# Performance work log

Hardware: AMD Instinct MI355X
Metric: run time of the kernel (lower is better)

Reference implementation:

```python
import jax, jax.numpy as jnp
import numpy as np

B, S, ENC_U, DEC_U, IN_DIM = 128, 1024, 1024, 1024, 64


def setup_inputs() -> dict:
    key = jax.random.key(0)
    ks = jax.random.split(key, 16)
    g = lambda k, shape, fan_in: jax.random.normal(k, shape, jnp.float32) / np.sqrt(fan_in)
    inp = {
        'x': jax.random.normal(ks[0], (B, 1, IN_DIM), jnp.float32),
        'hidden': jax.random.normal(ks[1], (B, DEC_U), jnp.float32),
        'enc_output': jax.random.normal(ks[2], (B, S, ENC_U), jnp.float32),
        # attention params
        'W1': g(ks[3], (ENC_U, DEC_U), ENC_U), 'b1': jnp.zeros((DEC_U,), jnp.float32),
        'W2': g(ks[4], (DEC_U, DEC_U), DEC_U), 'b2': jnp.zeros((DEC_U,), jnp.float32),
        'V': g(ks[5], (DEC_U, 1), DEC_U), 'bV': jnp.zeros((1,), jnp.float32),
        # GRU params (keras gate order: z, r, h); input to GRU is [context; x] -> ENC_U+IN_DIM
        'Wk': g(ks[6], (ENC_U + IN_DIM, 3 * DEC_U), ENC_U + IN_DIM),
        'Wr': g(ks[7], (DEC_U, 3 * DEC_U), DEC_U),
        'bg': jnp.zeros((3 * DEC_U,), jnp.float32),
        # output projection
        'Wfc': g(ks[8], (DEC_U, IN_DIM), DEC_U), 'bfc': jnp.zeros((IN_DIM,), jnp.float32),
    }
    return inp


def reference(x, hidden, enc_output, W1, b1, W2, b2, V, bV, Wk, Wr, bg, Wfc, bfc):
    U = hidden.shape[-1]
    # --- Bahdanau additive attention ---
    # score: (B, S, 1)
    feat = jnp.tanh(enc_output @ W1 + b1 + (hidden @ W2 + b2)[:, None, :])
    score = feat @ V + bV
    attention_weights = jax.nn.softmax(score, axis=1)            # (B, S, 1)
    context = jnp.sum(attention_weights * enc_output, axis=1)    # (B, ENC_U)
    # --- concat context with decoder input (single step) ---
    gin = jnp.concatenate([context, x[:, 0, :]], axis=-1)        # (B, ENC_U+IN_DIM)
    # --- one GRU cell step (reset_after=False, gate order z,r,h) ---
    xg = gin @ Wk + bg                                           # (B, 3U)
    z = jax.nn.sigmoid(xg[:, :U] + hidden @ Wr[:, :U])
    r = jax.nn.sigmoid(xg[:, U:2 * U] + hidden @ Wr[:, U:2 * U])
    hh = jnp.tanh(xg[:, 2 * U:] + (r * hidden) @ Wr[:, 2 * U:])
    state = z * hidden + (1.0 - z) * hh                          # (B, U)
    # return_sequences output with T=1 reshaped to (B, U) then fc
    out = state @ Wfc + bfc                                      # (B, IN_DIM)
    return out, state, attention_weights
```

## Files before the change

kernel.cpp:

```cpp
#include <hip/hip_runtime.h>
#include <cstdint>

#define B_  128
#define S_  1024
#define U_  1024
#define IN_ 64

typedef unsigned short u16;
typedef __attribute__((ext_vector_type(8))) short short8v;
typedef __attribute__((ext_vector_type(4))) float f32x4;

__device__ __forceinline__ u16 f2bf(float f) {
  uint32_t u = __builtin_bit_cast(uint32_t, f);
  u += 0x7fffu + ((u >> 16) & 1u);
  return (u16)(u >> 16);
}
__device__ __forceinline__ float bf2f(u16 h) {
  uint32_t u = ((uint32_t)h) << 16;
  return __builtin_bit_cast(float, u);
}
__device__ __forceinline__ float fast_tanh(float x) {
  float e = __expf(2.0f * x);
  return 1.0f - 2.0f * __builtin_amdgcn_rcpf(e + 1.0f);
}

__global__ void conv_enc_k(const float* __restrict__ in, u16* __restrict__ out) {
  size_t tid = (size_t)blockIdx.x * blockDim.x + threadIdx.x;
  size_t stride = (size_t)gridDim.x * blockDim.x;
  const size_t n8 = (size_t)B_ * S_ * U_ / 8;
  for (size_t p = tid; p < n8; p += stride) {
    const float* src = in + p * 8;
    float4 a = *(const float4*)src;
    float4 b = *(const float4*)(src + 4);
    short8v h;
    h[0] = (short)f2bf(a.x); h[1] = (short)f2bf(a.y);
    h[2] = (short)f2bf(a.z); h[3] = (short)f2bf(a.w);
    h[4] = (short)f2bf(b.x); h[5] = (short)f2bf(b.y);
    h[6] = (short)f2bf(b.z); h[7] = (short)f2bf(b.w);
    *(short8v*)(out + p * 8) = h;
  }
}

__global__ void conv_w1t_k(const float* __restrict__ W1, u16* __restrict__ w1t) {
  __shared__ float tile[32][33];
  int tx = threadIdx.x & 31, tg = threadIdx.x >> 5;
  int nb = blockIdx.x << 5, kb = blockIdx.y << 5;
#pragma unroll
  for (int i = 0; i < 4; ++i)
    tile[tg + i * 8][tx] = W1[(size_t)(kb + tg + i * 8) * U_ + nb + tx];
  __syncthreads();
#pragma unroll
  for (int i = 0; i < 4; ++i)
    w1t[(size_t)(nb + tg + i * 8) * U_ + kb + tx] = f2bf(tile[tx][tg + i * 8]);
}

__global__ __launch_bounds__(512, 2) void score_gemm2_k(
    const u16* __restrict__ encb, const u16* __restrict__ w1t,
    const float* __restrict__ hb, const float* __restrict__ b1,
    const float* __restrict__ b2, const float* __restrict__ Vv,
    float* __restrict__ score)
{
  __shared__ __align__(16) char lds[131072];
  const int tid  = threadIdx.x;
  const int lane = tid & 63;
  const int wid  = tid >> 6;
  const int wm = wid >> 2, wn = wid & 3;
  const int r16 = lane & 15, g4 = lane >> 4;

  int bid = blockIdx.x;
  int logical = (bid & 7) * 256 + (bid >> 3);
  const int row0 = (logical >> 2) << 8;
  const int n0   = (logical & 3) << 8;

  const int cx   = (g4 ^ ((r16 >> 1) & 3)) << 4;
  const int aoff = wm * 8192 + r16 * 64 + cx;
  const int boff = 16384 + wn * 4096 + r16 * 64 + cx;
  const int qA   = wid << 1;

  f32x4 acc[8][4] = {};

  auto stage = [&](int tk) {
    const int base = (tk & 3) << 15;
    const int kk = tk << 5;
#pragma unroll
    for (int i = 0; i < 2; ++i) {
      int q = qA + i;
      int cg = (q << 6) + lane;
      int row = cg >> 2, c = cg & 3;
      int j = c ^ ((row >> 1) & 3);
      const u16* srcA = encb + (((size_t)(row0 + row)) << 10) + kk + (j << 3);
      __builtin_amdgcn_global_load_lds(
          (const __attribute__((address_space(1))) void*)srcA,
          (__attribute__((address_space(3))) void*)(lds + base + (q << 10)), 16, 0, 0);
      const u16* srcB = w1t + (((size_t)(n0 + row)) << 10) + kk + (j << 3);
      __builtin_amdgcn_global_load_lds(
          (const __attribute__((address_space(1))) void*)srcB,
          (__attribute__((address_space(3))) void*)(lds + base + 16384 + (q << 10)), 16, 0, 0);
    }
  };

  auto compute = [&](int tk) {
    const char* base = lds + ((tk & 3) << 15);
    short8v af[8], bf[4];
#pragma unroll
    for (int mi = 0; mi < 8; ++mi)
      af[mi] = *(const short8v*)(base + aoff + mi * 1024);
#pragma unroll
    for (int ni = 0; ni < 4; ++ni)
      bf[ni] = *(const short8v*)(base + boff + ni * 1024);
    __builtin_amdgcn_s_setprio(1);
#pragma unroll
    for (int mi = 0; mi < 8; ++mi)
#pragma unroll
      for (int ni = 0; ni < 4; ++ni)
        acc[mi][ni] = __builtin_amdgcn_mfma_f32_16x16x32_bf16(af[mi], bf[ni], acc[mi][ni], 0, 0, 0);
    __builtin_amdgcn_s_setprio(0);
  };

  stage(0); stage(1); stage(2);
  for (int t = 0; t < 30; ++t) {
    asm volatile("s_waitcnt vmcnt(8)" ::: "memory");
    __builtin_amdgcn_s_barrier();
    __builtin_amdgcn_sched_barrier(0);
    if (t <= 28) stage(t + 3);
    compute(t);
  }
  asm volatile("s_waitcnt vmcnt(4)" ::: "memory");
  __builtin_amdgcn_s_barrier();
  compute(30);
  asm volatile("s_waitcnt vmcnt(0)" ::: "memory");
  __builtin_amdgcn_s_barrier();
  compute(31);

  const int b = row0 >> 10;
  float vv[4], hbv[4];
#pragma unroll
  for (int ni = 0; ni < 4; ++ni) {
    int col = n0 + (wn << 6) + (ni << 4) + r16;
    vv[ni]  = Vv[col];
    hbv[ni] = hb[(b << 10) + col] + b1[col] + b2[col];
  }
  float rowsum[8][4];
#pragma unroll
  for (int mi = 0; mi < 8; ++mi)
#pragma unroll
    for (int j = 0; j < 4; ++j) rowsum[mi][j] = 0.0f;
#pragma unroll
  for (int mi = 0; mi < 8; ++mi)
#pragma unroll
    for (int ni = 0; ni < 4; ++ni)
#pragma unroll
      for (int j = 0; j < 4; ++j)
        rowsum[mi][j] += fast_tanh(acc[mi][ni][j] + hbv[ni]) * vv[ni];
#pragma unroll
  for (int mi = 0; mi < 8; ++mi)
#pragma unroll
    for (int j = 0; j < 4; ++j) {
      float rs = rowsum[mi][j];
      rs += __shfl_xor(rs, 1);
      rs += __shfl_xor(rs, 2);
      rs += __shfl_xor(rs, 4);
      rs += __shfl_xor(rs, 8);
      if (r16 == 0)
        atomicAdd(score + row0 + (wm << 7) + (mi << 4) + (g4 << 2) + j, rs);
    }
}

__global__ __launch_bounds__(256) void score_gemm_f32_k(
    const float* __restrict__ encf, const u16* __restrict__ w1t,
    const float* __restrict__ hb, const float* __restrict__ b1,
    const float* __restrict__ b2, const float* __restrict__ Vv,
    float* __restrict__ score)
{
  __shared__ __align__(16) char lds[32768];
  const int tid  = threadIdx.x;
  const int lane = tid & 63;
  const int wid  = tid >> 6;
  const int wm = wid >> 1, wn = wid & 1;
  const int r16 = lane & 15, g4 = lane >> 4;
  int bid = blockIdx.x;
  int logical = (bid & 7) * 1024 + (bid >> 3);
  const int row0 = (logical >> 3) << 7;
  const int n0   = (logical & 7) << 7;
  f32x4 acc[4][4] = {};
  for (int kk = 0; kk < U_; kk += 64) {
#pragma unroll
    for (int qi = 0; qi < 4; ++qi) {
      int q = 16 + wid * 4 + qi;
      int n = ((q - 16) << 3) + (lane >> 3);
      int c = lane & 7;
      int j = c ^ (n & 7);
      const u16* src = w1t + (((size_t)(n0 + n)) << 10) + kk + (j << 3);
      __builtin_amdgcn_global_load_lds(
          (const __attribute__((address_space(1))) void*)src,
          (__attribute__((address_space(3))) void*)(lds + (q << 10)), 16, 0, 0);
    }
#pragma unroll
    for (int i = 0; i < 4; ++i) {
      int cg = tid * 4 + i;
      int r = cg >> 3, c = cg & 7;
      int j = c ^ (r & 7);
      const float* g = encf + (((size_t)(row0 + r)) << 10) + kk + (j << 3);
      float4 a = *(const float4*)g;
      float4 b = *(const float4*)(g + 4);
      short8v h;
      h[0] = (short)f2bf(a.x); h[1] = (short)f2bf(a.y);
      h[2] = (short)f2bf(a.z); h[3] = (short)f2bf(a.w);
      h[4] = (short)f2bf(b.x); h[5] = (short)f2bf(b.y);
      h[6] = (short)f2bf(b.z); h[7] = (short)f2bf(b.w);
      *(short8v*)(lds + (cg << 4)) = h;
    }
    __syncthreads();
#pragma unroll
    for (int ks = 0; ks < 2; ++ks) {
      short8v af[4], bf[4];
#pragma unroll
      for (int mi = 0; mi < 4; ++mi) {
        int row = (wm << 6) + (mi << 4) + r16;
        int jx = (ks << 2) + g4;
        af[mi] = *(const short8v*)(lds + (row << 7) + ((jx ^ (row & 7)) << 4));
      }
#pragma unroll
      for (int ni = 0; ni < 4; ++ni) {
        int n = (wn << 6) + (ni << 4) + r16;
        int jx = (ks << 2) + g4;
        bf[ni] = *(const short8v*)(lds + 16384 + (n << 7) + ((jx ^ (n & 7)) << 4));
      }
#pragma unroll
      for (int mi = 0; mi < 4; ++mi)
#pragma unroll
        for (int ni = 0; ni < 4; ++ni)
          acc[mi][ni] = __builtin_amdgcn_mfma_f32_16x16x32_bf16(af[mi], bf[ni], acc[mi][ni], 0, 0, 0);
    }
    __syncthreads();
  }
  const int b = row0 >> 10;
  float vv[4], hbv[4];
#pragma unroll
  for (int ni = 0; ni < 4; ++ni) {
    int col = n0 + (wn << 6) + (ni << 4) + r16;
    vv[ni]  = Vv[col];
    hbv[ni] = hb[(b << 10) + col] + b1[col] + b2[col];
  }
  float rowsum[4][4];
#pragma unroll
  for (int mi = 0; mi < 4; ++mi)
#pragma unroll
    for (int j = 0; j < 4; ++j) rowsum[mi][j] = 0.0f;
#pragma unroll
  for (int mi = 0; mi < 4; ++mi)
#pragma unroll
    for (int ni = 0; ni < 4; ++ni)
#pragma unroll
      for (int j = 0; j < 4; ++j)
        rowsum[mi][j] += fast_tanh(acc[mi][ni][j] + hbv[ni]) * vv[ni];
#pragma unroll
  for (int mi = 0; mi < 4; ++mi)
#pragma unroll
    for (int j = 0; j < 4; ++j) {
      float rs = rowsum[mi][j];
      rs += __shfl_xor(rs, 1);
      rs += __shfl_xor(rs, 2);
      rs += __shfl_xor(rs, 4);
      rs += __shfl_xor(rs, 8);
      if (r16 == 0)
        atomicAdd(score + row0 + (wm << 6) + (mi << 4) + (g4 << 2) + j, rs);
    }
}

__global__ void softmax_k(const float* __restrict__ score, float* __restrict__ attn) {
  __shared__ float red[8];
  int b = blockIdx.x, t = threadIdx.x;
  float4 v = ((const float4*)(score + ((size_t)b << 10)))[t];
  float m = fmaxf(fmaxf(v.x, v.y), fmaxf(v.z, v.w));
  for (int o = 1; o < 64; o <<= 1) m = fmaxf(m, __shfl_xor(m, o));
  if ((t & 63) == 0) red[t >> 6] = m;
  __syncthreads();
  m = fmaxf(fmaxf(red[0], red[1]), fmaxf(red[2], red[3]));
  float e0 = expf(v.x - m), e1 = expf(v.y - m), e2 = expf(v.z - m), e3 = expf(v.w - m);
  float s = e0 + e1 + e2 + e3;
  for (int o = 1; o < 64; o <<= 1) s += __shfl_xor(s, o);
  if ((t & 63) == 0) red[4 + (t >> 6)] = s;
  __syncthreads();
  s = red[4] + red[5] + red[6] + red[7];
  float inv = 1.0f / s;
  float4 o4; o4.x = e0 * inv; o4.y = e1 * inv; o4.z = e2 * inv; o4.w = e3 * inv;
  ((float4*)(attn + ((size_t)b << 10)))[t] = o4;
}

template<bool ABF16>
__global__ void context_k(const void* __restrict__ encp, const float* __restrict__ attn,
                          float* __restrict__ gin) {
  __shared__ float aw[128];
  int b = blockIdx.x >> 3, sc = blockIdx.x & 7, t = threadIdx.x;
  if (t < 128) aw[t] = attn[((size_t)b << 10) + sc * 128 + t];
  __syncthreads();
  float a0 = 0.f, a1 = 0.f, a2 = 0.f, a3 = 0.f;
  size_t base = ((size_t)b << 20) + ((size_t)(sc * 128) << 10);
  for (int s = 0; s < 128; ++s) {
    float w = aw[s];
    if (ABF16) {
      ushort4 e = *(const ushort4*)((const u16*)encp + base + ((size_t)s << 10) + t * 4);
      a0 += w * bf2f(e.x); a1 += w * bf2f(e.y); a2 += w * bf2f(e.z); a3 += w * bf2f(e.w);
    } else {
      float4 e = *(const float4*)((const float*)encp + base + ((size_t)s << 10) + t * 4);
      a0 += w * e.x; a1 += w * e.y; a2 += w * e.z; a3 += w * e.w;
    }
  }
  float* g = gin + (size_t)b * 1088 + t * 4;
  atomicAdd(g + 0, a0); atomicAdd(g + 1, a1); atomicAdd(g + 2, a2); atomicAdd(g + 3, a3);
}

__global__ void ginx_k(const float* __restrict__ x, float* __restrict__ gin) {
  int i = blockIdx.x * 256 + threadIdx.x;
  int b = i >> 6, c = i & 63;
  gin[(size_t)b * 1088 + 1024 + c] = x[i];
}

__global__ __launch_bounds__(256) void gemm_splitk_k(
    const float* __restrict__ A, int lda,
    const float* __restrict__ W, int ldw,
    float* __restrict__ C, int ldc)
{
  __shared__ float As[64][68];
  __shared__ float Bs[64][64];
  int t = threadIdx.x;
  int m0 = blockIdx.x << 6, n0 = blockIdx.y << 6, k0 = blockIdx.z << 6;
#pragma unroll
  for (int q = 0; q < 4; ++q) {
    int cidx = q * 256 + t;
    int m = cidx >> 4, c4 = cidx & 15;
    float4 v = *(const float4*)(A + (size_t)(m0 + m) * lda + k0 + (c4 << 2));
    As[m][(c4 << 2) + 0] = v.x; As[m][(c4 << 2) + 1] = v.y;
    As[m][(c4 << 2) + 2] = v.z; As[m][(c4 << 2) + 3] = v.w;
  }
#pragma unroll
  for (int q = 0; q < 4; ++q) {
    int cidx = q * 256 + t;
    int k = cidx >> 4, nn = cidx & 15;
    *(float4*)&Bs[k][nn << 2] =
        *(const float4*)(W + (size_t)(k0 + k) * ldw + n0 + (nn << 2));
  }
  __syncthreads();
  int tx = t & 15, ty = t >> 4;
  float acc[4][4] = {};
#pragma unroll 8
  for (int k = 0; k < 64; ++k) {
    float a0 = As[(ty << 2) + 0][k], a1 = As[(ty << 2) + 1][k];
    float a2 = As[(ty << 2) + 2][k], a3 = As[(ty << 2) + 3][k];
    float4 bv = *(const float4*)&Bs[k][tx << 2];
    acc[0][0] += a0 * bv.x; acc[0][1] += a0 * bv.y; acc[0][2] += a0 * bv.z; acc[0][3] += a0 * bv.w;
    acc[1][0] += a1 * bv.x; acc[1][1] += a1 * bv.y; acc[1][2] += a1 * bv.z; acc[1][3] += a1 * bv.w;
    acc[2][0] += a2 * bv.x; acc[2][1] += a2 * bv.y; acc[2][2] += a2 * bv.z; acc[2][3] += a2 * bv.w;
    acc[3][0] += a3 * bv.x; acc[3][1] += a3 * bv.y; acc[3][2] += a3 * bv.z; acc[3][3] += a3 * bv.w;
  }
  int col = n0 + (tx << 2);
#pragma unroll
  for (int i = 0; i < 4; ++i) {
    int row = m0 + (ty << 2) + i;
#pragma unroll
    for (int j = 0; j < 4; ++j)
      atomicAdd(C + (size_t)row * ldc + col + j, acc[i][j]);
  }
}

__global__ void zr_k(const float* __restrict__ xg, const float* __restrict__ hr,
                     const float* __restrict__ hid, const float* __restrict__ bg,
                     float* __restrict__ z, float* __restrict__ rh) {
  int i = blockIdx.x * 256 + threadIdx.x;
  int b = i >> 10, n = i & 1023;
  float zv = xg[(size_t)b * 3072 + n] + bg[n] + hr[(size_t)b * 2048 + n];
  float rv = xg[(size_t)b * 3072 + 1024 + n] + bg[1024 + n] + hr[(size_t)b * 2048 + 1024 + n];
  zv = 1.0f / (1.0f + expf(-zv));
  rv = 1.0f / (1.0f + expf(-rv));
  z[i] = zv;
  rh[i] = rv * hid[i];
}

__global__ void state_ep_k(const float* __restrict__ hh, const float* __restrict__ xg,
                           const float* __restrict__ bg, const float* __restrict__ z,
                           const float* __restrict__ hid, float* __restrict__ state) {
  int i = blockIdx.x * 256 + threadIdx.x;
  int b = i >> 10, n = i & 1023;
  float val = hh[i] + xg[(size_t)b * 3072 + 2048 + n] + bg[2048 + n];
  float th = tanhf(val);
  float zv = z[i];
  state[i] = zv * hid[i] + (1.0f - zv) * th;
}

__global__ void out_ep_k(float* __restrict__ out, const float* __restrict__ bfc) {
  int i = blockIdx.x * 256 + threadIdx.x;
  out[i] += bfc[i & 63];
}

extern "C" void kernel_launch(void* const* d_in, const int* in_sizes, int n_in,
                              void* d_out, int out_size, void* d_ws, size_t ws_size,
                              hipStream_t stream) {
  const float* x    = (const float*)d_in[0];
  const float* hid  = (const float*)d_in[1];
  const float* enc  = (const float*)d_in[2];
  const float* W1   = (const float*)d_in[3];
  const float* b1   = (const float*)d_in[4];
  const float* W2   = (const float*)d_in[5];
  const float* b2   = (const float*)d_in[6];
  const float* Vv   = (const float*)d_in[7];
  const float* Wk   = (const float*)d_in[9];
  const float* Wr   = (const float*)d_in[10];
  const float* bg   = (const float*)d_in[11];
  const float* Wfc  = (const float*)d_in[12];
  const float* bfc  = (const float*)d_in[13];

  float* out       = (float*)d_out;
  float* state_out = out + 8192;
  float* attn_out  = out + 8192 + 131072;

  char* ws = (char*)d_ws;
  u16*   w1t   = (u16*)(ws + 0);
  float* hb    = (float*)(ws + 2097152);
  float* score = (float*)(ws + 2621440);
  float* gin   = (float*)(ws + 3145728);
  float* xg    = (float*)(ws + 3702784);
  float* hr    = (float*)(ws + 5275648);
  float* hh    = (float*)(ws + 6324224);
  float* z     = (float*)(ws + 6848512);
  float* rh    = (float*)(ws + 7372800);
  u16*   enc16 = (u16*)(ws + 8388608);
  const bool pathA = ws_size >= (8388608ULL + 268435456ULL);

  hipMemsetAsync(ws + 2097152, 0, 6848512 - 2097152, stream);
  hipMemsetAsync(out, 0, 32768, stream);

  conv_w1t_k<<<dim3(32, 32), 256, 0, stream>>>(W1, w1t);
  if (pathA) conv_enc_k<<<4096, 256, 0, stream>>>(enc, enc16);

  gemm_splitk_k<<<dim3(2, 16, 16), 256, 0, stream>>>(hid, 1024, W2, 1024, hb, 1024);

  if (pathA)
    score_gemm2_k<<<2048, 512, 0, stream>>>(enc16, w1t, hb, b1, b2, Vv, score);
  else
    score_gemm_f32_k<<<8192, 256, 0, stream>>>(enc, w1t, hb, b1, b2, Vv, score);

  softmax_k<<<128, 256, 0, stream>>>(score, attn_out);

  if (pathA) context_k<true><<<1024, 256, 0, stream>>>(enc16, attn_out, gin);
  else       context_k<false><<<1024, 256, 0, stream>>>(enc, attn_out, gin);
  ginx_k<<<32, 256, 0, stream>>>(x, gin);

  gemm_splitk_k<<<dim3(2, 48, 17), 256, 0, stream>>>(gin, 1088, Wk, 3072, xg, 3072);
  gemm_splitk_k<<<dim3(2, 32, 16), 256, 0, stream>>>(hid, 1024, Wr, 3072, hr, 2048);
  zr_k<<<512, 256, 0, stream>>>(xg, hr, hid, bg, z, rh);
  gemm_splitk_k<<<dim3(2, 16, 16), 256, 0, stream>>>(rh, 1024, Wr + 2048, 3072, hh, 1024);
  state_ep_k<<<512, 256, 0, stream>>>(hh, xg, bg, z, hid, state_out);
  gemm_splitk_k<<<dim3(2, 1, 16), 256, 0, stream>>>(state_out, 1024, Wfc, 64, out, 64);
  out_ep_k<<<32, 256, 0, stream>>>(out, bfc);
}
```

Before: 817.7 us.

## Double-buffer LDS fragments in score GEMM to overlap LDS reads with MFMA

Restructures the score GEMM main loop so register fragments for the next k-tile are read from LDS while MFMAs run on the current tile, using two ping-pong fragment register sets. The launch-bounds occupancy hint drops from two blocks per CU to one to make room for the extra registers. This hides LDS read latency inside the wave at the cost of less cross-wave latency hiding. The vmcnt waits and the prologue and epilogue are rewritten to match the new schedule.

```diff
diff --git a/kernel.cpp b/kernel.cpp
--- a/kernel.cpp
+++ b/kernel.cpp
@@ -54,7 +54,7 @@
     w1t[(size_t)(nb + tg + i * 8) * U_ + kb + tx] = f2bf(tile[tx][tg + i * 8]);
 }
 
-__global__ __launch_bounds__(512, 2) void score_gemm2_k(
+__global__ __launch_bounds__(512, 1) void score_gemm2_k(
     const u16* __restrict__ encb, const u16* __restrict__ w1t,
     const float* __restrict__ hb, const float* __restrict__ b1,
     const float* __restrict__ b2, const float* __restrict__ Vv,
@@ -78,6 +78,7 @@
   const int qA   = wid << 1;
 
   f32x4 acc[8][4] = {};
+  short8v afA[8], bfA[4], afB[8], bfB[4];
 
   auto stage = [&](int tk) {
     const int base = (tk & 3) << 15;
@@ -99,15 +100,17 @@
     }
   };
 
-  auto compute = [&](int tk) {
+  auto loadfrag = [&](short8v (&af)[8], short8v (&bf)[4], int tk) {
     const char* base = lds + ((tk & 3) << 15);
-    short8v af[8], bf[4];
 #pragma unroll
     for (int mi = 0; mi < 8; ++mi)
       af[mi] = *(const short8v*)(base + aoff + mi * 1024);
 #pragma unroll
     for (int ni = 0; ni < 4; ++ni)
       bf[ni] = *(const short8v*)(base + boff + ni * 1024);
+  };
+
+  auto compute = [&](short8v (&af)[8], short8v (&bf)[4]) {
     __builtin_amdgcn_s_setprio(1);
 #pragma unroll
     for (int mi = 0; mi < 8; ++mi)
@@ -118,19 +121,43 @@
   };
 
   stage(0); stage(1); stage(2);
-  for (int t = 0; t < 30; ++t) {
-    asm volatile("s_waitcnt vmcnt(8)" ::: "memory");
+  asm volatile("s_waitcnt vmcnt(8)" ::: "memory");
+  __builtin_amdgcn_s_barrier();
+  __builtin_amdgcn_sched_barrier(0);
+  loadfrag(afA, bfA, 0);
+
+  for (int t = 0; t < 28; t += 2) {
+    asm volatile("s_waitcnt vmcnt(4)" ::: "memory");
     __builtin_amdgcn_s_barrier();
     __builtin_amdgcn_sched_barrier(0);
-    if (t <= 28) stage(t + 3);
-    compute(t);
+    stage(t + 3);
+    loadfrag(afB, bfB, t + 1);
+    compute(afA, bfA);
+
+    asm volatile("s_waitcnt vmcnt(4)" ::: "memory");
+    __builtin_amdgcn_s_barrier();
+    __builtin_amdgcn_sched_barrier(0);
+    stage(t + 4);
+    loadfrag(afA, bfA, t + 2);
+    compute(afB, bfB);
   }
   asm volatile("s_waitcnt vmcnt(4)" ::: "memory");
   __builtin_amdgcn_s_barrier();
-  compute(30);
+  __builtin_amdgcn_sched_barrier(0);
+  stage(31);
+  loadfrag(afB, bfB, 29);
+  compute(afA, bfA);
+  asm volatile("s_waitcnt vmcnt(4)" ::: "memory");
+  __builtin_amdgcn_s_barrier();
+  __builtin_amdgcn_sched_barrier(0);
+  loadfrag(afA, bfA, 30);
+  compute(afB, bfB);
   asm volatile("s_waitcnt vmcnt(0)" ::: "memory");
   __builtin_amdgcn_s_barrier();
-  compute(31);
+  __builtin_amdgcn_sched_barrier(0);
+  loadfrag(afB, bfB, 31);
+  compute(afA, bfA);
+  compute(afB, bfB);
 
   const int b = row0 >> 10;
   float vv[4], hbv[4];
```

Measured after the change: 821.6 us. Within noise of the previous version (+0.5%).

## Restructure score GEMM main loop into double-buffered phased pipeline with one block per CU

Applied to the files above, without the earlier changes.

The score GEMM main loop is rebuilt as a two-buffer, 64-wide K-step pipeline. Each step is split into four phases that interleave LDS fragment reads, async global-to-LDS staging of the next tile, and MFMA bursts, with barriers around each phase. Occupancy is dropped to one 512-thread block per CU so the compiler gets more registers for the software-pipelined schedule. Global addresses are precomputed per thread to cut address arithmetic in the loop. The extra barriers and the loss of a second resident block may reduce latency hiding.

```diff
diff --git a/kernel.cpp b/kernel.cpp
--- a/kernel.cpp
+++ b/kernel.cpp
@@ -54,7 +54,7 @@
     w1t[(size_t)(nb + tg + i * 8) * U_ + kb + tx] = f2bf(tile[tx][tg + i * 8]);
 }
 
-__global__ __launch_bounds__(512, 2) void score_gemm2_k(
+__global__ __launch_bounds__(512, 1) void score_gemm2_k(
     const u16* __restrict__ encb, const u16* __restrict__ w1t,
     const float* __restrict__ hb, const float* __restrict__ b1,
     const float* __restrict__ b2, const float* __restrict__ Vv,
@@ -73,64 +73,85 @@
   const int n0   = (logical & 3) << 8;
 
   const int cx   = (g4 ^ ((r16 >> 1) & 3)) << 4;
-  const int aoff = wm * 8192 + r16 * 64 + cx;
-  const int boff = 16384 + wn * 4096 + r16 * 64 + cx;
-  const int qA   = wid << 1;
+  const int arow = (wm * 128 + r16) * 64 + cx;
+  const int brow = (wn * 64  + r16) * 64 + cx;
+
+  const int jsw  = (tid & 3) ^ ((tid >> 3) & 3);
+  const u16* pA0 = encb + (((size_t)(row0 + (tid >> 2))) << 10) + jsw * 8;
+  const u16* pA1 = pA0 + (size_t)128 * 1024;
+  const u16* pB0 = w1t  + (((size_t)(n0   + (tid >> 2))) << 10) + jsw * 8;
+  const u16* pB1 = pB0 + (size_t)128 * 1024;
 
   f32x4 acc[8][4] = {};
-
-  auto stage = [&](int tk) {
-    const int base = (tk & 3) << 15;
-    const int kk = tk << 5;
-#pragma unroll
-    for (int i = 0; i < 2; ++i) {
-      int q = qA + i;
-      int cg = (q << 6) + lane;
-      int row = cg >> 2, c = cg & 3;
-      int j = c ^ ((row >> 1) & 3);
-      const u16* srcA = encb + (((size_t)(row0 + row)) << 10) + kk + (j << 3);
-      __builtin_amdgcn_global_load_lds(
-          (const __attribute__((address_space(1))) void*)srcA,
-          (__attribute__((address_space(3))) void*)(lds + base + (q << 10)), 16, 0, 0);
-      const u16* srcB = w1t + (((size_t)(n0 + row)) << 10) + kk + (j << 3);
-      __builtin_amdgcn_global_load_lds(
-          (const __attribute__((address_space(1))) void*)srcB,
-          (__attribute__((address_space(3))) void*)(lds + base + 16384 + (q << 10)), 16, 0, 0);
-    }
-  };
-
-  auto compute = [&](int tk) {
-    const char* base = lds + ((tk & 3) << 15);
-    short8v af[8], bf[4];
-#pragma unroll
-    for (int mi = 0; mi < 8; ++mi)
-      af[mi] = *(const short8v*)(base + aoff + mi * 1024);
-#pragma unroll
-    for (int ni = 0; ni < 4; ++ni)
-      bf[ni] = *(const short8v*)(base + boff + ni * 1024);
-    __builtin_amdgcn_s_setprio(1);
-#pragma unroll
-    for (int mi = 0; mi < 8; ++mi)
-#pragma unroll
-      for (int ni = 0; ni < 4; ++ni)
-        acc[mi][ni] = __builtin_amdgcn_mfma_f32_16x16x32_bf16(af[mi], bf[ni], acc[mi][ni], 0, 0, 0);
-    __builtin_amdgcn_s_setprio(0);
-  };
-
-  stage(0); stage(1); stage(2);
-  for (int t = 0; t < 30; ++t) {
-    asm volatile("s_waitcnt vmcnt(8)" ::: "memory");
-    __builtin_amdgcn_s_barrier();
-    __builtin_amdgcn_sched_barrier(0);
-    if (t <= 28) stage(t + 3);
-    compute(t);
+  short8v bfr[4];
+
+#define STAGE(PTR0, PTR1, REGOFF, KOFF) do {                                   \
+    const int _wb = _np + (REGOFF) + (wid << 10);                              \
+    __builtin_amdgcn_global_load_lds(                                          \
+        (const __attribute__((address_space(1))) void*)((PTR0) + (KOFF)),      \
+        (__attribute__((address_space(3))) void*)(lds + _wb), 16, 0, 0);       \
+    __builtin_amdgcn_global_load_lds(                                          \
+        (const __attribute__((address_space(1))) void*)((PTR1) + (KOFF)),      \
+        (__attribute__((address_space(3))) void*)(lds + _wb + 8192), 16, 0, 0);\
+  } while (0)
+
+#define PHASE(M2, KS, DO_STAGE, SPTR0, SPTR1, SREG, VM) do {                   \
+    short8v af[4];                                                             \
+    { const char* _ab = lds + _pb + (KS) * 16384;                              \
+      _Pragma("unroll")                                                        \
+      for (int mi = 0; mi < 4; ++mi)                                           \
+        af[mi] = *(const short8v*)(_ab + arow + ((M2) * 4 + mi) * 1024); }     \
+    if ((M2) == 0) {                                                           \
+      const char* _bb = lds + _pb + 32768 + (KS) * 16384;                      \
+      _Pragma("unroll")                                                        \
+      for (int ni = 0; ni < 4; ++ni)                                           \
+        bfr[ni] = *(const short8v*)(_bb + brow + ni * 1024); }                 \
+    if (DO_STAGE) { STAGE(SPTR0, SPTR1, SREG, _kbase + (KS) * 32); }           \
+    if ((VM) == 4)      asm volatile("s_waitcnt vmcnt(4)" ::: "memory");       \
+    else if ((VM) == 0) asm volatile("s_waitcnt vmcnt(0)" ::: "memory");       \
+    __builtin_amdgcn_s_barrier();                                              \
+    asm volatile("s_waitcnt lgkmcnt(0)" ::: "memory");                         \
+    __builtin_amdgcn_sched_barrier(0);                                         \
+    __builtin_amdgcn_s_setprio(1);                                             \
+    _Pragma("unroll")                                                          \
+    for (int mi = 0; mi < 4; ++mi)                                             \
+      _Pragma("unroll")                                                        \
+      for (int ni = 0; ni < 4; ++ni)                                           \
+        acc[(M2) * 4 + mi][ni] = __builtin_amdgcn_mfma_f32_16x16x32_bf16(      \
+            af[mi], bfr[ni], acc[(M2) * 4 + mi][ni], 0, 0, 0);                 \
+    __builtin_amdgcn_s_setprio(0);                                             \
+    __builtin_amdgcn_s_barrier();                                              \
+  } while (0)
+
+  {
+    const int _np = 0;
+    STAGE(pA0, pA1, 0,     0);
+    STAGE(pB0, pB1, 32768, 0);
+    STAGE(pA0, pA1, 16384, 32);
+    STAGE(pB0, pB1, 49152, 32);
   }
   asm volatile("s_waitcnt vmcnt(4)" ::: "memory");
   __builtin_amdgcn_s_barrier();
-  compute(30);
-  asm volatile("s_waitcnt vmcnt(0)" ::: "memory");
-  __builtin_amdgcn_s_barrier();
-  compute(31);
+
+  for (int t = 0; t < 15; ++t) {
+    const int _pb = (t & 1) << 16;
+    const int _np = _pb ^ 65536;
+    const size_t _kbase = (size_t)(t + 1) << 6;
+    PHASE(0, 0, 1, pA0, pA1, 0,     -1);
+    PHASE(1, 0, 1, pB0, pB1, 32768,  4);
+    PHASE(0, 1, 1, pA0, pA1, 16384, -1);
+    PHASE(1, 1, 1, pB0, pB1, 49152,  4);
+  }
+  {
+    const int _pb = (15 & 1) << 16;
+    const int _np = 0; const size_t _kbase = 0; (void)_np; (void)_kbase;
+    PHASE(0, 0, 0, pA0, pA1, 0, -1);
+    PHASE(1, 0, 0, pA0, pA1, 0,  0);
+    PHASE(0, 1, 0, pA0, pA1, 0, -1);
+    PHASE(1, 1, 0, pA0, pA1, 0, -1);
+  }
+#undef PHASE
+#undef STAGE
 
   const int b = row0 >> 10;
   float vv[4], hbv[4];
```

New measurement: 807.6 us. No clear change (-1.2%).

## Restructure score GEMM to 256x128 tiles with double-buffered 8-wave-style ping-pong

Applied to the files above, without the earlier changes.

The score GEMM moves from 512-thread blocks with 256x256 tiles and a 4-deep LDS ring to 256-thread blocks with 256x128 tiles and a two-buffer LDS scheme (48KB). Each k-step is split into two half-MFMA phases, with barriers placed so the next tile's global->LDS load overlaps compute. The smaller LDS footprint allows more resident blocks per CU. In exchange each tile carries a lower compute-to-load ratio and more barriers per step.

```diff
diff --git a/kernel.cpp b/kernel.cpp
--- a/kernel.cpp
+++ b/kernel.cpp
@@ -54,83 +54,100 @@
     w1t[(size_t)(nb + tg + i * 8) * U_ + kb + tx] = f2bf(tile[tx][tg + i * 8]);
 }
 
-__global__ __launch_bounds__(512, 2) void score_gemm2_k(
+__global__ __launch_bounds__(256, 2) void score_gemm3_k(
     const u16* __restrict__ encb, const u16* __restrict__ w1t,
     const float* __restrict__ hb, const float* __restrict__ b1,
     const float* __restrict__ b2, const float* __restrict__ Vv,
     float* __restrict__ score)
 {
-  __shared__ __align__(16) char lds[131072];
+  __shared__ __align__(16) char lds[49152];
   const int tid  = threadIdx.x;
   const int lane = tid & 63;
   const int wid  = tid >> 6;
-  const int wm = wid >> 2, wn = wid & 3;
+  const int wm = wid >> 1, wn = wid & 1;
   const int r16 = lane & 15, g4 = lane >> 4;
 
   int bid = blockIdx.x;
-  int logical = (bid & 7) * 256 + (bid >> 3);
-  const int row0 = (logical >> 2) << 8;
-  const int n0   = (logical & 3) << 8;
+  int logical = (bid & 7) * 512 + (bid >> 3);
+  const int row0 = (logical >> 3) << 8;
+  const int n0   = (logical & 7) << 7;
 
   const int cx   = (g4 ^ ((r16 >> 1) & 3)) << 4;
-  const int aoff = wm * 8192 + r16 * 64 + cx;
-  const int boff = 16384 + wn * 4096 + r16 * 64 + cx;
-  const int qA   = wid << 1;
+  const int arow = wm * 8192 + r16 * 64 + cx;
+  const int brow = 16384 + wn * 4096 + r16 * 64 + cx;
+
+  const int jsw  = (tid & 3) ^ ((tid >> 3) & 3);
+  const u16* pA  = encb + (((size_t)(row0 + (tid >> 2))) << 10) + jsw * 8;
+  const u16* pB  = w1t  + (((size_t)(n0   + (tid >> 2))) << 10) + jsw * 8;
 
   f32x4 acc[8][4] = {};
-
-  auto stage = [&](int tk) {
-    const int base = (tk & 3) << 15;
-    const int kk = tk << 5;
-#pragma unroll
-    for (int i = 0; i < 2; ++i) {
-      int q = qA + i;
-      int cg = (q << 6) + lane;
-      int row = cg >> 2, c = cg & 3;
-      int j = c ^ ((row >> 1) & 3);
-      const u16* srcA = encb + (((size_t)(row0 + row)) << 10) + kk + (j << 3);
-      __builtin_amdgcn_global_load_lds(
-          (const __attribute__((address_space(1))) void*)srcA,
-          (__attribute__((address_space(3))) void*)(lds + base + (q << 10)), 16, 0, 0);
-      const u16* srcB = w1t + (((size_t)(n0 + row)) << 10) + kk + (j << 3);
-      __builtin_amdgcn_global_load_lds(
-          (const __attribute__((address_space(1))) void*)srcB,
-          (__attribute__((address_space(3))) void*)(lds + base + 16384 + (q << 10)), 16, 0, 0);
-    }
-  };
-
-  auto compute = [&](int tk) {
-    const char* base = lds + ((tk & 3) << 15);
-    short8v af[8], bf[4];
-#pragma unroll
-    for (int mi = 0; mi < 8; ++mi)
-      af[mi] = *(const short8v*)(base + aoff + mi * 1024);
-#pragma unroll
-    for (int ni = 0; ni < 4; ++ni)
-      bf[ni] = *(const short8v*)(base + boff + ni * 1024);
-    __builtin_amdgcn_s_setprio(1);
-#pragma unroll
-    for (int mi = 0; mi < 8; ++mi)
-#pragma unroll
-      for (int ni = 0; ni < 4; ++ni)
-        acc[mi][ni] = __builtin_amdgcn_mfma_f32_16x16x32_bf16(af[mi], bf[ni], acc[mi][ni], 0, 0, 0);
-    __builtin_amdgcn_s_setprio(0);
-  };
-
-  stage(0); stage(1); stage(2);
-  for (int t = 0; t < 30; ++t) {
-    asm volatile("s_waitcnt vmcnt(8)" ::: "memory");
-    __builtin_amdgcn_s_barrier();
-    __builtin_amdgcn_sched_barrier(0);
-    if (t <= 28) stage(t + 3);
-    compute(t);
-  }
-  asm volatile("s_waitcnt vmcnt(4)" ::: "memory");
-  __builtin_amdgcn_s_barrier();
-  compute(30);
+  short8v bfr[4];
+
+#define STAGE6(KOFF) do {                                                      \
+    const int _wb = _np + (wid << 10);                                         \
+    _Pragma("unroll")                                                          \
+    for (int i = 0; i < 4; ++i)                                                \
+      __builtin_amdgcn_global_load_lds(                                        \
+          (const __attribute__((address_space(1))) void*)(pA + (size_t)i * 65536 + (KOFF)), \
+          (__attribute__((address_space(3))) void*)(lds + _wb + i * 4096), 16, 0, 0); \
+    _Pragma("unroll")                                                          \
+    for (int i = 0; i < 2; ++i)                                                \
+      __builtin_amdgcn_global_load_lds(                                        \
+          (const __attribute__((address_space(1))) void*)(pB + (size_t)i * 65536 + (KOFF)), \
+          (__attribute__((address_space(3))) void*)(lds + _wb + 16384 + i * 4096), 16, 0, 0); \
+  } while (0)
+
+#define MFMA16(M2, AF) do {                                                    \
+    __builtin_amdgcn_s_setprio(1);                                             \
+    _Pragma("unroll")                                                          \
+    for (int mi = 0; mi < 4; ++mi)                                             \
+      _Pragma("unroll")                                                        \
+      for (int ni = 0; ni < 4; ++ni)                                           \
+        acc[(M2) * 4 + mi][ni] = __builtin_amdgcn_mfma_f32_16x16x32_bf16(      \
+            (AF)[mi], bfr[ni], acc[(M2) * 4 + mi][ni], 0, 0, 0);               \
+    __builtin_amdgcn_s_setprio(0);                                             \
+  } while (0)
+
+  {
+    const int _np = 0;
+    STAGE6(0);
+  }
   asm volatile("s_waitcnt vmcnt(0)" ::: "memory");
   __builtin_amdgcn_s_barrier();
-  compute(31);
+
+  for (int t = 0; t < 32; ++t) {
+    const int _pb = (t & 1) * 24576;
+    const int _np = _pb ^ 24576;
+    {
+      short8v af[4];
+      const char* _ab = lds + _pb;
+#pragma unroll
+      for (int mi = 0; mi < 4; ++mi)
+        af[mi] = *(const short8v*)(_ab + arow + mi * 1024);
+#pragma unroll
+      for (int ni = 0; ni < 4; ++ni)
+        bfr[ni] = *(const short8v*)(_ab + brow + ni * 1024);
+      if (t < 31) { STAGE6((size_t)(t + 1) << 5); }
+      __builtin_amdgcn_s_barrier();
+      asm volatile("s_waitcnt lgkmcnt(0)" ::: "memory");
+      __builtin_amdgcn_sched_barrier(0);
+      MFMA16(0, af);
+    }
+    {
+      short8v af[4];
+      const char* _ab = lds + _pb;
+#pragma unroll
+      for (int mi = 0; mi < 4; ++mi)
+        af[mi] = *(const short8v*)(_ab + arow + (4 + mi) * 1024);
+      if (t < 31) asm volatile("s_waitcnt vmcnt(0)" ::: "memory");
+      __builtin_amdgcn_s_barrier();
+      asm volatile("s_waitcnt lgkmcnt(0)" ::: "memory");
+      __builtin_amdgcn_sched_barrier(0);
+      MFMA16(1, af);
+    }
+  }
+#undef STAGE6
+#undef MFMA16
 
   const int b = row0 >> 10;
   float vv[4], hbv[4];
@@ -436,7 +453,7 @@
   gemm_splitk_k<<<dim3(2, 16, 16), 256, 0, stream>>>(hid, 1024, W2, 1024, hb, 1024);
 
   if (pathA)
-    score_gemm2_k<<<2048, 512, 0, stream>>>(enc16, w1t, hb, b1, b2, Vv, score);
+    score_gemm3_k<<<4096, 256, 0, stream>>>(enc16, w1t, hb, b1, b2, Vv, score);
   else
     score_gemm_f32_k<<<8192, 256, 0, stream>>>(enc, w1t, hb, b1, b2, Vv, score);
 
```

Result: slower. 840.8 us (+2.8%).
